# Optimization experiments

Hardware: AMD Instinct MI355X
Metric: run time of the kernel (lower is better)

## Reference

```python
import jax, jax.numpy as jnp
import numpy as np
from jax import lax

N, CIN, H, W = 128, 1024, 14, 14
CF, TH = 128, 128          # cv_filter, te_hidden
HP, GT, FP, A = 256, 256, 256, 32


def setup_inputs() -> dict:
    key = jax.random.key(0)
    ks = jax.random.split(key, 12)
    s = 0.05
    return {
        "image": jax.random.normal(ks[0], (N, CIN, H, W), jnp.float32),
        "code": jax.random.normal(ks[1], (N, TH), jnp.float32),
        "conv_w": jax.random.normal(ks[2], (CF, CIN, 3, 3), jnp.float32) * 0.02,
        "conv_b": jnp.zeros((CF,), jnp.float32),
        "hp_w0": jax.random.normal(ks[3], (CF + 2 + TH, HP), jnp.float32) * s,
        "hp_b0": jnp.zeros((HP,), jnp.float32),
        "hp_w1": jax.random.normal(ks[4], (HP, 1), jnp.float32) * s,
        "hp_b1": jnp.zeros((1,), jnp.float32),
        "gt_w0": jax.random.normal(ks[5], ((CF + 2) * 2 + TH, GT), jnp.float32) * s,
        "gt_b0": jnp.zeros((GT,), jnp.float32),
        "gt_w1": jax.random.normal(ks[6], (GT, GT), jnp.float32) * s,
        "gt_b1": jnp.zeros((GT,), jnp.float32),
        "fp_w0": jax.random.normal(ks[7], (GT, FP), jnp.float32) * s,
        "fp_b0": jnp.zeros((FP,), jnp.float32),
        "fp_w1": jax.random.normal(ks[8], (FP, A), jnp.float32) * s,
        "fp_b1": jnp.zeros((A,), jnp.float32),
    }


def _sarn(image, code, conv_w, conv_b, hp_w0, hp_b0, hp_w1, hp_b1,
          gt_w0, gt_b0, gt_w1, gt_b1, fp_w0, fp_b0, fp_w1, fp_b1):
    # visual_resize: 3x3 conv, stride 1, pad 1 (NCHW)
    x = lax.conv_general_dilated(image, conv_w, (1, 1), "SAME",
                                 dimension_numbers=("NCHW", "OIHW", "NCHW"))
    x = x + conv_b[None, :, None, None]                       # [n, cf, h, w]
    n, c, h, w = x.shape
    o = h * w
    # sarn_encode: append x/y coordinate channels and question code
    xc = jnp.broadcast_to(jnp.linspace(-1.0, 1.0, h).reshape(1, 1, h, 1), (n, 1, h, w))
    yc = jnp.broadcast_to(jnp.linspace(-1.0, 1.0, w).reshape(1, 1, 1, w), (n, 1, h, w))
    coord = jnp.concatenate([x, xc, yc], axis=1)              # [n, cf+2, h, w]
    q = jnp.broadcast_to(code[:, :, None, None], (n, code.shape[1], h, w))
    qenc = jnp.concatenate([coord, q], axis=1)                # [n, cf+2+th, h, w]
    ce = coord.reshape(n, c + 2, o).transpose(0, 2, 1)        # [n, o, cf+2]
    qe = qenc.reshape(n, -1, o).transpose(0, 2, 1)            # [n, o, cf+2+th]
    # h_psi: per-object attention logit
    a = jax.nn.relu(jnp.einsum("nod,dh->noh", qe, hp_w0) + hp_b0)
    att = jnp.einsum("noh,hk->nok", a, hp_w1) + hp_b1         # [n, o, 1]
    # sarn_pair: softmax select a single soft object, pair with every object
    sel = jax.nn.softmax(att[..., 0], axis=1)                 # [n, o]
    selected = jnp.einsum("no,nod->nd", sel, ce)              # [n, cf+2]
    pairs = jnp.concatenate(
        [qe, jnp.broadcast_to(selected[:, None, :], ce.shape)], axis=2)  # [n, o, 2*(cf+2)+th]
    # g_theta MLP + sum over objects
    g = jax.nn.relu(jnp.einsum("nop,pg->nog", pairs, gt_w0) + gt_b0)
    g = jax.nn.relu(jnp.einsum("nog,gk->nok", g, gt_w1) + gt_b1)
    relations = g.sum(axis=1)                                 # [n, gt]
    # f_phi MLP -> answer logits
    f = jax.nn.relu(relations @ fp_w0 + fp_b0)
    return f @ fp_w1 + fp_b1                                  # [n, a_size]


def reference(image, code, conv_w, conv_b, hp_w0, hp_b0, hp_w1, hp_b1,
              gt_w0, gt_b0, gt_w1, gt_b1, fp_w0, fp_b0, fp_w1, fp_b1):
    return _sarn(image, code, conv_w, conv_b, hp_w0, hp_b0, hp_w1, hp_b1,
                 gt_w0, gt_b0, gt_w1, gt_b1, fp_w0, fp_b0, fp_w1, fp_b1)
```

## Files before the change

### kernel.cpp

```cpp
#include <hip/hip_runtime.h>
#include <stdint.h>

typedef unsigned short u16;
typedef __bf16 bf16x8 __attribute__((ext_vector_type(8)));
typedef float f32x4 __attribute__((ext_vector_type(4)));

__device__ __forceinline__ u16 f2b(float f) {
  union { float f; uint32_t u; } v; v.f = f;
  uint32_t r = v.u + 0x7fffu + ((v.u >> 16) & 1u);
  return (u16)(r >> 16);
}
__device__ __forceinline__ float b2f(u16 b) {
  union { float f; uint32_t u; } v; v.u = ((uint32_t)b) << 16;
  return v.f;
}
__device__ __forceinline__ void g2l16(const void* g, void* l) {
  __builtin_amdgcn_global_load_lds(
      (const __attribute__((address_space(1))) void*)g,
      (__attribute__((address_space(3))) void*)l, 16, 0, 0);
}

#define N_SAMP 128
#define OPAD   224
#define ROWS   (N_SAMP * OPAD)
#define KQ     160

__global__ __launch_bounds__(256) void prep_weights(
    const float* __restrict__ conv_w, const float* __restrict__ hp_w0,
    const float* __restrict__ gt_w0, const float* __restrict__ gt_w1,
    const float* __restrict__ hp_b0, const float* __restrict__ code,
    u16* __restrict__ W2, u16* __restrict__ hp_w0t,
    u16* __restrict__ gt_w0t, u16* __restrict__ gt_w1t,
    float* __restrict__ biasHP) {
  int idx = blockIdx.x * 256 + threadIdx.x;
  const int nW2 = 9 * 128 * 1024;
  const int nHP = 256 * KQ;
  const int nGT0 = 256 * KQ;
  const int nGT1 = 256 * 256;
  if (idx < nW2) {
    int s = idx / 131072; int r = idx & 131071;
    int cf = r >> 10; int cin = r & 1023;
    W2[idx] = f2b(conv_w[(cf * 1024 + cin) * 9 + s]);
    return;
  }
  idx -= nW2;
  if (idx < nHP) {
    int nn = idx / KQ, kk = idx % KQ;
    hp_w0t[nn * KQ + kk] = (kk < 130) ? f2b(hp_w0[kk * 256 + nn]) : (u16)0;
    return;
  }
  idx -= nHP;
  if (idx < nGT0) {
    int nn = idx / KQ, kk = idx % KQ;
    gt_w0t[nn * KQ + kk] = (kk < 130) ? f2b(gt_w0[kk * 256 + nn]) : (u16)0;
    return;
  }
  idx -= nGT0;
  if (idx < nGT1) {
    int nn = idx >> 8, kk = idx & 255;
    gt_w1t[nn * 256 + kk] = f2b(gt_w1[kk * 256 + nn]);
    return;
  }
  idx -= nGT1;
  {
    int n = idx >> 8, t = idx & 255;
    float acc = hp_b0[t];
    for (int d = 0; d < 128; ++d)
      acc += code[n * 128 + d] * hp_w0[(130 + d) * 256 + t];
    biasHP[n * 256 + t] = acc;
  }
}

__global__ __launch_bounds__(256) void prep_img(const float* __restrict__ image,
                                                u16* __restrict__ imgT) {
  __shared__ float t[64][197];
  int n = blockIdx.x >> 4;
  int cin0 = (blockIdx.x & 15) * 64;
  const float* src = image + ((size_t)n * 1024 + cin0) * 196;
  for (int e = threadIdx.x; e < 64 * 196; e += 256) {
    int c = e / 196, sp = e % 196;
    t[c][sp] = src[c * 196 + sp];
  }
  __syncthreads();
  int w = threadIdx.x >> 6, lane = threadIdx.x & 63;
  for (int i = 0; i < 64; ++i) {
    int spg = i * 4 + w;
    int gy = spg >> 4, gx = spg & 15;
    float v = 0.f;
    if (gy >= 1 && gy <= 14 && gx >= 1 && gx <= 14) v = t[lane][(gy - 1) * 14 + (gx - 1)];
    imgT[(((size_t)(n * 256 + spg)) << 10) + cin0 + lane] = f2b(v);
  }
}

__global__ __launch_bounds__(256) void fill_qe(u16* __restrict__ qeb) {
  int idx = blockIdx.x * 256 + threadIdx.x;
  if (idx < ROWS * 8) {
    int row = idx >> 3, qd = idx & 7;
    int o = row % 224;
    ushort4 v = {0, 0, 0, 0};
    if (o < 196 && qd == 0) {
      int y = o / 14, x = o % 14;
      v.x = f2b(-1.f + 2.f * y / 13.f);
      v.y = f2b(-1.f + 2.f * x / 13.f);
    }
    *(ushort4*)(qeb + (size_t)row * KQ + 128 + qd * 4) = v;
    return;
  }
  idx -= ROWS * 8;
  int pr = idx >> 5, qd = idx & 31;
  int row = (pr / 28) * 224 + 196 + (pr % 28);
  *(ushort4*)(qeb + (size_t)row * KQ + qd * 4) = (ushort4){0, 0, 0, 0};
}

__global__ __launch_bounds__(256) void conv_gemm(
    const u16* __restrict__ imgT, const u16* __restrict__ W2,
    float* __restrict__ convAcc) {
  __shared__ __align__(16) u16 lA[112 * 64];
  __shared__ __align__(16) u16 lB[128 * 64];
  int tid = threadIdx.x, lane = tid & 63, w = tid >> 6;
  int wg = blockIdx.x;
  int xcd = wg & 7, grp = wg >> 3;
  int n = ((grp / 6) << 3) | xcd;
  int r6 = grp % 6;
  int oh = r6 / 3, ks = r6 % 3;
  int oBase = oh * 112;
  size_t nBase = (size_t)n << 8;
  int rowIn = lane >> 3;
  int cA = ((lane & 7) ^ rowIn) << 3;

  int yxA[4];
  for (int ii = 0; ii < 4; ++ii) {
    int t = w + ii * 4;
    int o = oBase + t * 8 + rowIn;
    bool valid = o < 196;
    int y = o / 14, x = o - y * 14;
    yxA[ii] = valid ? (y * 16 + x) : 0;
  }

  f32x4 acc[7][2];
#pragma unroll
  for (int mt = 0; mt < 7; ++mt)
#pragma unroll
    for (int j = 0; j < 2; ++j) acc[mt][j] = (f32x4){0.f, 0.f, 0.f, 0.f};

  int l = lane & 15, q = lane >> 4;
  for (int si = 0; si < 3; ++si) {
    int s = ks * 3 + si;
    int off = (s / 3) * 16 + (s % 3);
    const u16* Ws = W2 + ((size_t)(s * 128) << 10);
    for (int cb = 0; cb < 16; ++cb) {
      int k0 = cb << 6;
      __syncthreads();
      g2l16(imgT + ((nBase + (size_t)(yxA[0] + off)) << 10) + k0 + cA, &lA[(w) * 512]);
      g2l16(imgT + ((nBase + (size_t)(yxA[1] + off)) << 10) + k0 + cA, &lA[(w + 4) * 512]);
      g2l16(imgT + ((nBase + (size_t)(yxA[2] + off)) << 10) + k0 + cA, &lA[(w + 8) * 512]);
      if (w < 2)
        g2l16(imgT + ((nBase + (size_t)(yxA[3] + off)) << 10) + k0 + cA, &lA[(w + 12) * 512]);
#pragma unroll
      for (int ii = 0; ii < 4; ++ii) {
        int t = w + ii * 4;
        g2l16(Ws + ((size_t)(t * 8 + rowIn) << 10) + k0 + cA, &lB[t * 512]);
      }
      __syncthreads();
#pragma unroll
      for (int kk = 0; kk < 2; ++kk) {
        int co = ((((kk << 2) | q) ^ (l & 7)) << 3);
        bf16x8 af[7];
#pragma unroll
        for (int mt = 0; mt < 7; ++mt)
          af[mt] = *(const bf16x8*)&lA[(mt * 16 + l) * 64 + co];
#pragma unroll
        for (int jj = 0; jj < 2; ++jj) {
          bf16x8 bb = *(const bf16x8*)&lB[(w * 32 + jj * 16 + l) * 64 + co];
#pragma unroll
          for (int mt = 0; mt < 7; ++mt)
            acc[mt][jj] = __builtin_amdgcn_mfma_f32_16x16x32_bf16(af[mt], bb, acc[mt][jj], 0, 0, 0);
        }
      }
    }
  }
#pragma unroll
  for (int mt = 0; mt < 7; ++mt) {
    int o = oBase + mt * 16 + q * 4;
#pragma unroll
    for (int r4 = 0; r4 < 4; ++r4) {
      if (o + r4 < 196) {
        float* dst = convAcc + (size_t)(n * 224 + o + r4) * 128 + w * 32 + l;
        atomicAdd(dst, acc[mt][0][r4]);
        atomicAdd(dst + 16, acc[mt][1][r4]);
      }
    }
  }
}

__global__ __launch_bounds__(256) void conv_fix(
    const float* __restrict__ convAcc, const float* __restrict__ conv_b,
    u16* __restrict__ qeb) {
  int idx = blockIdx.x * 256 + threadIdx.x;
  int row196 = idx >> 5;
  int c0 = (idx & 31) << 2;
  int n = row196 / 196, o = row196 - n * 196;
  size_t row = (size_t)(n * 224 + o);
  const float4 v = *(const float4*)(convAcc + (row << 7) + c0);
  const float4 b = *(const float4*)(conv_b + c0);
  ushort4 pk;
  pk.x = f2b(v.x + b.x); pk.y = f2b(v.y + b.y);
  pk.z = f2b(v.z + b.z); pk.w = f2b(v.w + b.w);
  *(ushort4*)(qeb + row * KQ + c0) = pk;
}

template <int MODE, int KP, int KC>
__global__ __launch_bounds__(256) void gemm_kernel(
    const u16* __restrict__ A, const u16* __restrict__ Bt,
    const float* __restrict__ bias, const float* __restrict__ vec,
    float* __restrict__ outF, u16* __restrict__ outB) {
  __shared__ __align__(16) u16 lA[2][128 * 32];
  __shared__ __align__(16) u16 lB[2][128 * 32];
  int tid = threadIdx.x, lane = tid & 63, w = tid >> 6;
  int bx = blockIdx.x, by = blockIdx.y;
  int r0 = bx * 112;
  int cBase = by * 128;
  int kb = (((lane & 3) ^ ((lane >> 3) & 3)) << 3);
  int rA0 = r0 + w * 16 + (lane >> 2);
  int rA1 = r0 + (w + 4) * 16 + (lane >> 2);
  const u16* gA0 = A + (size_t)rA0 * KP + kb;
  const u16* gA1 = A + (size_t)rA1 * KP + kb;
  int cB0 = cBase + w * 16 + (lane >> 2);
  int cB1 = cBase + (w + 4) * 16 + (lane >> 2);
  const u16* gB0 = Bt + (size_t)cB0 * KP + kb;
  const u16* gB1 = Bt + (size_t)cB1 * KP + kb;

  f32x4 acc[7][2];
#pragma unroll
  for (int mt = 0; mt < 7; ++mt)
#pragma unroll
    for (int j = 0; j < 2; ++j) acc[mt][j] = (f32x4){0.f, 0.f, 0.f, 0.f};
  int colW = w * 32;
  int l = lane & 15, q = lane >> 4;
  int co = ((q ^ ((l >> 1) & 3)) << 3);

  auto STAGE = [&](int buf, int cb) {
    g2l16(gA0 + cb * 32, &lA[buf][w * 512]);
    g2l16(gA1 + cb * 32, &lA[buf][(w + 4) * 512]);
    g2l16(gB0 + cb * 32, &lB[buf][w * 512]);
    g2l16(gB1 + cb * 32, &lB[buf][(w + 4) * 512]);
  };

  auto COMPUTE = [&](int cur) {
    bf16x8 af[7];
#pragma unroll
    for (int mt = 0; mt < 7; ++mt)
      af[mt] = *(const bf16x8*)&lA[cur][(mt * 16 + l) * 32 + co];
#pragma unroll
    for (int j = 0; j < 2; ++j) {
      bf16x8 bfr = *(const bf16x8*)&lB[cur][(colW + j * 16 + l) * 32 + co];
#pragma unroll
      for (int mt = 0; mt < 7; ++mt)
        acc[mt][j] = __builtin_amdgcn_mfma_f32_16x16x32_bf16(af[mt], bfr, acc[mt][j], 0, 0, 0);
    }
  };

  STAGE(0, 0);
#pragma unroll
  for (int it = 0; it < KC - 1; ++it) {
    STAGE((it & 1) ^ 1, it + 1);
    asm volatile("s_waitcnt vmcnt(4)" ::: "memory");
    __builtin_amdgcn_s_barrier();
    __builtin_amdgcn_sched_barrier(0);
    COMPUTE(it & 1);
    __builtin_amdgcn_s_barrier();
    __builtin_amdgcn_sched_barrier(0);
  }
  asm volatile("s_waitcnt vmcnt(0)" ::: "memory");
  __builtin_amdgcn_s_barrier();
  __builtin_amdgcn_sched_barrier(0);
  COMPUTE((KC - 1) & 1);

  int q4 = lane >> 4, c = lane & 15;
  if (MODE == 0) {
    int n = bx >> 1;
    float attp[7][4];
#pragma unroll
    for (int mt = 0; mt < 7; ++mt)
#pragma unroll
      for (int r = 0; r < 4; ++r) attp[mt][r] = 0.f;
#pragma unroll
    for (int j = 0; j < 2; ++j) {
      int col = cBase + colW + j * 16 + c;
      float b0 = bias[n * 256 + col], w1 = vec[col];
#pragma unroll
      for (int mt = 0; mt < 7; ++mt)
#pragma unroll
        for (int r = 0; r < 4; ++r) {
          float v = fmaxf(acc[mt][j][r] + b0, 0.f);
          attp[mt][r] += v * w1;
        }
    }
#pragma unroll
    for (int mt = 0; mt < 7; ++mt)
#pragma unroll
      for (int r = 0; r < 4; ++r) {
        float p = attp[mt][r];
        p += __shfl_xor(p, 1, 64);
        p += __shfl_xor(p, 2, 64);
        p += __shfl_xor(p, 4, 64);
        p += __shfl_xor(p, 8, 64);
        if (c == 0) atomicAdd(&outF[r0 + mt * 16 + q4 * 4 + r], p);
      }
  } else if (MODE == 1) {
    int n = bx >> 1;
#pragma unroll
    for (int mt = 0; mt < 7; ++mt)
#pragma unroll
      for (int j = 0; j < 2; ++j) {
        int col = cBase + colW + j * 16 + c;
        float b = bias[n * 256 + col];
#pragma unroll
        for (int r = 0; r < 4; ++r) {
          int row = r0 + mt * 16 + q4 * 4 + r;
          outB[(size_t)row * 256 + col] = f2b(fmaxf(acc[mt][j][r] + b, 0.f));
        }
      }
  } else {
    int n = bx >> 1;
    int ob = (bx & 1) * 112;
#pragma unroll
    for (int j = 0; j < 2; ++j) {
      int col = cBase + colW + j * 16 + c;
      float b = bias[col];
      float sum = 0.f;
#pragma unroll
      for (int mt = 0; mt < 7; ++mt)
#pragma unroll
        for (int r = 0; r < 4; ++r) {
          int o = ob + mt * 16 + q4 * 4 + r;
          if (o < 196) sum += fmaxf(acc[mt][j][r] + b, 0.f);
        }
      sum += __shfl_xor(sum, 16, 64);
      sum += __shfl_xor(sum, 32, 64);
      if (q4 == 0) atomicAdd(&outF[n * 256 + col], sum);
    }
  }
}

__global__ __launch_bounds__(256) void sel_kernel(
    const float* __restrict__ att, const u16* __restrict__ qeb,
    const float* __restrict__ gt_w0, const float* __restrict__ gt_b0,
    const float* __restrict__ code, float* __restrict__ bias2) {
  int n = blockIdx.x, t = threadIdx.x;
  int w = t >> 6, lane = t & 63;
  __shared__ u16 sq[196][130];
  __shared__ float sm[196];
  __shared__ float sel[130];
  __shared__ float red[8];
  const u16* base = qeb + (size_t)n * 224 * KQ;
  for (int o = w; o < 196; o += 4) {
    const u16* rowp = base + (size_t)o * KQ;
    for (int c = lane; c < 130; c += 64) sq[o][c] = rowp[c];
  }
  float a = (t < 196) ? att[n * 224 + t] : -1e30f;
  float m = a;
  for (int mask = 1; mask < 64; mask <<= 1) m = fmaxf(m, __shfl_xor(m, mask, 64));
  if (lane == 0) red[w] = m;
  __syncthreads();
  float M = fmaxf(fmaxf(red[0], red[1]), fmaxf(red[2], red[3]));
  float e = (t < 196) ? expf(a - M) : 0.f;
  float sAcc = e;
  for (int mask = 1; mask < 64; mask <<= 1) sAcc += __shfl_xor(sAcc, mask, 64);
  if (lane == 0) red[4 + w] = sAcc;
  __syncthreads();
  float S = red[4] + red[5] + red[6] + red[7];
  if (t < 196) sm[t] = e / S;
  __syncthreads();
  if (t < 130) {
    float acc = 0.f;
    for (int o = 0; o < 196; ++o) acc += sm[o] * b2f(sq[o][t]);
    sel[t] = acc;
  }
  __syncthreads();
  float acc2 = gt_b0[t];
  for (int d = 0; d < 130; ++d) acc2 += sel[d] * gt_w0[(258 + d) * 256 + t];
  for (int d = 0; d < 128; ++d) acc2 += code[n * 128 + d] * gt_w0[(130 + d) * 256 + t];
  bias2[n * 256 + t] = acc2;
}

__global__ __launch_bounds__(256) void fphi(
    const float* __restrict__ relations, const float* __restrict__ fp_w0,
    const float* __restrict__ fp_b0, const float* __restrict__ fp_w1,
    const float* __restrict__ fp_b1, float* __restrict__ out) {
  int n = blockIdx.x, t = threadIdx.x;
  __shared__ float rel[256];
  __shared__ float f[256];
  rel[t] = relations[n * 256 + t];
  __syncthreads();
  float acc = fp_b0[t];
  for (int k = 0; k < 256; ++k) acc += rel[k] * fp_w0[k * 256 + t];
  f[t] = fmaxf(acc, 0.f);
  __syncthreads();
  if (t < 32) {
    float o = fp_b1[0];
    for (int k = 0; k < 256; ++k) o += f[k] * fp_w1[k * 32 + t];
    out[n * 32 + t] = o;
  }
}

extern "C" void kernel_launch(void* const* d_in, const int* in_sizes, int n_in,
                              void* d_out, int out_size, void* d_ws, size_t ws_size,
                              hipStream_t stream) {
  const float* image = (const float*)d_in[0];
  const float* code = (const float*)d_in[1];
  const float* conv_w = (const float*)d_in[2];
  const float* conv_b = (const float*)d_in[3];
  const float* hp_w0 = (const float*)d_in[4];
  const float* hp_b0 = (const float*)d_in[5];
  const float* hp_w1 = (const float*)d_in[6];
  const float* gt_w0 = (const float*)d_in[8];
  const float* gt_b0 = (const float*)d_in[9];
  const float* gt_w1 = (const float*)d_in[10];
  const float* gt_b1 = (const float*)d_in[11];
  const float* fp_w0 = (const float*)d_in[12];
  const float* fp_b0 = (const float*)d_in[13];
  const float* fp_w1 = (const float*)d_in[14];
  const float* fp_b1 = (const float*)d_in[15];
  float* out = (float*)d_out;

  char* p = (char*)d_ws;
  u16* imgT = (u16*)p;   p += (size_t)128 * 256 * 1024 * 2;
  u16* W2 = (u16*)p;     p += (size_t)9 * 128 * 1024 * 2;
  u16* qeb = (u16*)p;    p += (size_t)ROWS * KQ * 2;
  u16* hp_w0t = (u16*)p; p += (size_t)256 * KQ * 2;
  u16* gt_w0t = (u16*)p; p += (size_t)256 * KQ * 2;
  u16* gt_w1t = (u16*)p; p += (size_t)256 * 256 * 2;
  float* att = (float*)p;    p += (size_t)ROWS * 4;
  float* bias2 = (float*)p;  p += (size_t)128 * 256 * 4;
  float* biasHP = (float*)p; p += (size_t)128 * 256 * 4;
  float* convAcc = (float*)p; p += (size_t)ROWS * 128 * 4;
  float* relations = (float*)p; p += (size_t)128 * 256 * 4;
  u16* g1 = (u16*)convAcc;

  hipMemsetAsync(att, 0, (size_t)ROWS * 4, stream);
  hipMemsetAsync(relations, 0, (size_t)128 * 256 * 4, stream);
  hipMemsetAsync(convAcc, 0, (size_t)ROWS * 128 * 4, stream);

  prep_weights<<<5312, 256, 0, stream>>>(conv_w, hp_w0, gt_w0, gt_w1, hp_b0, code,
                                         W2, hp_w0t, gt_w0t, gt_w1t, biasHP);
  prep_img<<<2048, 256, 0, stream>>>(image, imgT);
  fill_qe<<<1344, 256, 0, stream>>>(qeb);
  conv_gemm<<<768, 256, 0, stream>>>(imgT, W2, convAcc);
  conv_fix<<<3136, 256, 0, stream>>>(convAcc, conv_b, qeb);
  gemm_kernel<0, KQ, 5><<<dim3(256, 2), 256, 0, stream>>>(qeb, hp_w0t, biasHP, hp_w1, att, nullptr);
  sel_kernel<<<128, 256, 0, stream>>>(att, qeb, gt_w0, gt_b0, code, bias2);
  gemm_kernel<1, KQ, 5><<<dim3(256, 2), 256, 0, stream>>>(qeb, gt_w0t, bias2, nullptr, nullptr, g1);
  gemm_kernel<2, 256, 8><<<dim3(256, 2), 256, 0, stream>>>(g1, gt_w1t, gt_b1, nullptr, relations, nullptr);
  fphi<<<128, 256, 0, stream>>>(relations, fp_w0, fp_b0, fp_w1, fp_b1, out);
}
```

Before: 397.0 us.

## Merge prep kernels and memsets, coalesce weight and image repacking

```diff
diff --git a/kernel.cpp b/kernel.cpp
--- a/kernel.cpp
+++ b/kernel.cpp
@@ -25,50 +25,98 @@
 #define ROWS   (N_SAMP * OPAD)
 #define KQ     160
 
-__global__ __launch_bounds__(256) void prep_weights(
-    const float* __restrict__ conv_w, const float* __restrict__ hp_w0,
-    const float* __restrict__ gt_w0, const float* __restrict__ gt_w1,
-    const float* __restrict__ hp_b0, const float* __restrict__ code,
-    u16* __restrict__ W2, u16* __restrict__ hp_w0t,
-    u16* __restrict__ gt_w0t, u16* __restrict__ gt_w1t,
-    float* __restrict__ biasHP) {
+__global__ __launch_bounds__(256) void prep_w2(const float* __restrict__ conv_w,
+                                               u16* __restrict__ W2) {
+  __shared__ float ls[2304];
+  int p0 = blockIdx.x << 8;
+  int t = threadIdx.x;
+  const float* src = conv_w + (size_t)p0 * 9;
+#pragma unroll
+  for (int i = 0; i < 9; ++i) ls[t + i * 256] = src[t + i * 256];
+  __syncthreads();
+#pragma unroll
+  for (int s = 0; s < 9; ++s)
+    W2[s * 131072 + p0 + t] = f2b(ls[t * 9 + s]);
+}
+
+#define R_HP   40960
+#define R_GT0  40960
+#define R_GT1  65536
+#define R_BHP  32768
+#define R_BGT  32768
+#define R_QC   (ROWS * 8)
+#define R_QP   114688
+#define R_ATT  7168
+#define R_REL  8192
+#define R_CVA  917504
+__global__ __launch_bounds__(256) void init_misc(
+    const float* __restrict__ hp_w0, const float* __restrict__ gt_w0,
+    const float* __restrict__ gt_w1, const float* __restrict__ hp_b0,
+    const float* __restrict__ gt_b0, const float* __restrict__ code,
+    u16* __restrict__ hp_w0t, u16* __restrict__ gt_w0t, u16* __restrict__ gt_w1t,
+    float* __restrict__ biasHP, float* __restrict__ biasGT, u16* __restrict__ qeb,
+    float* __restrict__ att, float* __restrict__ relations,
+    float* __restrict__ convAcc) {
   int idx = blockIdx.x * 256 + threadIdx.x;
-  const int nW2 = 9 * 128 * 1024;
-  const int nHP = 256 * KQ;
-  const int nGT0 = 256 * KQ;
-  const int nGT1 = 256 * 256;
-  if (idx < nW2) {
-    int s = idx / 131072; int r = idx & 131071;
-    int cf = r >> 10; int cin = r & 1023;
-    W2[idx] = f2b(conv_w[(cf * 1024 + cin) * 9 + s]);
-    return;
-  }
-  idx -= nW2;
-  if (idx < nHP) {
+  if (idx < R_HP) {
     int nn = idx / KQ, kk = idx % KQ;
-    hp_w0t[nn * KQ + kk] = (kk < 130) ? f2b(hp_w0[kk * 256 + nn]) : (u16)0;
-    return;
-  }
-  idx -= nHP;
-  if (idx < nGT0) {
+    hp_w0t[idx] = (kk < 130) ? f2b(hp_w0[kk * 256 + nn]) : (u16)0;
+    return;
+  }
+  idx -= R_HP;
+  if (idx < R_GT0) {
     int nn = idx / KQ, kk = idx % KQ;
-    gt_w0t[nn * KQ + kk] = (kk < 130) ? f2b(gt_w0[kk * 256 + nn]) : (u16)0;
-    return;
-  }
-  idx -= nGT0;
-  if (idx < nGT1) {
+    gt_w0t[idx] = (kk < 130) ? f2b(gt_w0[kk * 256 + nn]) : (u16)0;
+    return;
+  }
+  idx -= R_GT0;
+  if (idx < R_GT1) {
     int nn = idx >> 8, kk = idx & 255;
-    gt_w1t[nn * 256 + kk] = f2b(gt_w1[kk * 256 + nn]);
-    return;
-  }
-  idx -= nGT1;
-  {
+    gt_w1t[idx] = f2b(gt_w1[kk * 256 + nn]);
+    return;
+  }
+  idx -= R_GT1;
+  if (idx < R_BHP) {
     int n = idx >> 8, t = idx & 255;
     float acc = hp_b0[t];
-    for (int d = 0; d < 128; ++d)
-      acc += code[n * 128 + d] * hp_w0[(130 + d) * 256 + t];
-    biasHP[n * 256 + t] = acc;
-  }
+    for (int d = 0; d < 128; ++d) acc += code[n * 128 + d] * hp_w0[(130 + d) * 256 + t];
+    biasHP[idx] = acc;
+    return;
+  }
+  idx -= R_BHP;
+  if (idx < R_BGT) {
+    int n = idx >> 8, t = idx & 255;
+    float acc = gt_b0[t];
+    for (int d = 0; d < 128; ++d) acc += code[n * 128 + d] * gt_w0[(130 + d) * 256 + t];
+    biasGT[idx] = acc;
+    return;
+  }
+  idx -= R_BGT;
+  if (idx < R_QC) {
+    int row = idx >> 3, qd = idx & 7;
+    int o = row % 224;
+    ushort4 v = {0, 0, 0, 0};
+    if (o < 196 && qd == 0) {
+      int y = o / 14, x = o % 14;
+      v.x = f2b(-1.f + 2.f * y / 13.f);
+      v.y = f2b(-1.f + 2.f * x / 13.f);
+    }
+    *(ushort4*)(qeb + (size_t)row * KQ + 128 + qd * 4) = v;
+    return;
+  }
+  idx -= R_QC;
+  if (idx < R_QP) {
+    int pr = idx >> 5, qd = idx & 31;
+    int row = (pr / 28) * 224 + 196 + (pr % 28);
+    *(ushort4*)(qeb + (size_t)row * KQ + qd * 4) = (ushort4){0, 0, 0, 0};
+    return;
+  }
+  idx -= R_QP;
+  if (idx < R_ATT) { *((float4*)att + idx) = (float4){0.f, 0.f, 0.f, 0.f}; return; }
+  idx -= R_ATT;
+  if (idx < R_REL) { *((float4*)relations + idx) = (float4){0.f, 0.f, 0.f, 0.f}; return; }
+  idx -= R_REL;
+  *((float4*)convAcc + idx) = (float4){0.f, 0.f, 0.f, 0.f};
 }
 
 __global__ __launch_bounds__(256) void prep_img(const float* __restrict__ image,
@@ -82,34 +130,24 @@
     t[c][sp] = src[c * 196 + sp];
   }
   __syncthreads();
-  int w = threadIdx.x >> 6, lane = threadIdx.x & 63;
-  for (int i = 0; i < 64; ++i) {
-    int spg = i * 4 + w;
+#pragma unroll
+  for (int i = 0; i < 8; ++i) {
+    int qid = threadIdx.x + i * 256;
+    int spg = qid >> 3, qd = qid & 7;
     int gy = spg >> 4, gx = spg & 15;
-    float v = 0.f;
-    if (gy >= 1 && gy <= 14 && gx >= 1 && gx <= 14) v = t[lane][(gy - 1) * 14 + (gx - 1)];
-    imgT[(((size_t)(n * 256 + spg)) << 10) + cin0 + lane] = f2b(v);
-  }
-}
-
-__global__ __launch_bounds__(256) void fill_qe(u16* __restrict__ qeb) {
-  int idx = blockIdx.x * 256 + threadIdx.x;
-  if (idx < ROWS * 8) {
-    int row = idx >> 3, qd = idx & 7;
-    int o = row % 224;
-    ushort4 v = {0, 0, 0, 0};
-    if (o < 196 && qd == 0) {
-      int y = o / 14, x = o % 14;
-      v.x = f2b(-1.f + 2.f * y / 13.f);
-      v.y = f2b(-1.f + 2.f * x / 13.f);
-    }
-    *(ushort4*)(qeb + (size_t)row * KQ + 128 + qd * 4) = v;
-    return;
-  }
-  idx -= ROWS * 8;
-  int pr = idx >> 5, qd = idx & 31;
-  int row = (pr / 28) * 224 + 196 + (pr % 28);
-  *(ushort4*)(qeb + (size_t)row * KQ + qd * 4) = (ushort4){0, 0, 0, 0};
+    uint4 pk = {0u, 0u, 0u, 0u};
+    if (gy >= 1 && gy <= 14 && gx >= 1 && gx <= 14) {
+      int sp = (gy - 1) * 14 + (gx - 1);
+      uint32_t vv[8];
+#pragma unroll
+      for (int j = 0; j < 8; ++j) vv[j] = f2b(t[qd * 8 + j][sp]);
+      pk.x = vv[0] | (vv[1] << 16);
+      pk.y = vv[2] | (vv[3] << 16);
+      pk.z = vv[4] | (vv[5] << 16);
+      pk.w = vv[6] | (vv[7] << 16);
+    }
+    *(uint4*)(imgT + (((size_t)(n * 256 + spg)) << 10) + cin0 + qd * 8) = pk;
+  }
 }
 
 __global__ __launch_bounds__(256) void conv_gemm(
@@ -345,8 +383,8 @@
 
 __global__ __launch_bounds__(256) void sel_kernel(
     const float* __restrict__ att, const u16* __restrict__ qeb,
-    const float* __restrict__ gt_w0, const float* __restrict__ gt_b0,
-    const float* __restrict__ code, float* __restrict__ bias2) {
+    const float* __restrict__ gt_w0, const float* __restrict__ biasGT,
+    float* __restrict__ bias2) {
   int n = blockIdx.x, t = threadIdx.x;
   int w = t >> 6, lane = t & 63;
   __shared__ u16 sq[196][130];
@@ -378,9 +416,8 @@
     sel[t] = acc;
   }
   __syncthreads();
-  float acc2 = gt_b0[t];
+  float acc2 = biasGT[n * 256 + t];
   for (int d = 0; d < 130; ++d) acc2 += sel[d] * gt_w0[(258 + d) * 256 + t];
-  for (int d = 0; d < 128; ++d) acc2 += code[n * 128 + d] * gt_w0[(130 + d) * 256 + t];
   bias2[n * 256 + t] = acc2;
 }
 
@@ -434,22 +471,20 @@
   float* att = (float*)p;    p += (size_t)ROWS * 4;
   float* bias2 = (float*)p;  p += (size_t)128 * 256 * 4;
   float* biasHP = (float*)p; p += (size_t)128 * 256 * 4;
+  float* biasGT = (float*)p; p += (size_t)128 * 256 * 4;
   float* convAcc = (float*)p; p += (size_t)ROWS * 128 * 4;
   float* relations = (float*)p; p += (size_t)128 * 256 * 4;
   u16* g1 = (u16*)convAcc;
 
-  hipMemsetAsync(att, 0, (size_t)ROWS * 4, stream);
-  hipMemsetAsync(relations, 0, (size_t)128 * 256 * 4, stream);
-  hipMemsetAsync(convAcc, 0, (size_t)ROWS * 128 * 4, stream);
-
-  prep_weights<<<5312, 256, 0, stream>>>(conv_w, hp_w0, gt_w0, gt_w1, hp_b0, code,
-                                         W2, hp_w0t, gt_w0t, gt_w1t, biasHP);
+  init_misc<<<5820, 256, 0, stream>>>(hp_w0, gt_w0, gt_w1, hp_b0, gt_b0, code,
+                                      hp_w0t, gt_w0t, gt_w1t, biasHP, biasGT, qeb,
+                                      att, relations, convAcc);
+  prep_w2<<<512, 256, 0, stream>>>(conv_w, W2);
   prep_img<<<2048, 256, 0, stream>>>(image, imgT);
-  fill_qe<<<1344, 256, 0, stream>>>(qeb);
   conv_gemm<<<768, 256, 0, stream>>>(imgT, W2, convAcc);
   conv_fix<<<3136, 256, 0, stream>>>(convAcc, conv_b, qeb);
   gemm_kernel<0, KQ, 5><<<dim3(256, 2), 256, 0, stream>>>(qeb, hp_w0t, biasHP, hp_w1, att, nullptr);
-  sel_kernel<<<128, 256, 0, stream>>>(att, qeb, gt_w0, gt_b0, code, bias2);
+  sel_kernel<<<128, 256, 0, stream>>>(att, qeb, gt_w0, biasGT, bias2);
   gemm_kernel<1, KQ, 5><<<dim3(256, 2), 256, 0, stream>>>(qeb, gt_w0t, bias2, nullptr, nullptr, g1);
   gemm_kernel<2, 256, 8><<<dim3(256, 2), 256, 0, stream>>>(g1, gt_w1t, gt_b1, nullptr, relations, nullptr);
   fphi<<<128, 256, 0, stream>>>(relations, fp_w0, fp_b0, fp_w1, fp_b1, out);
```

After: 381.8 us. 3.8% less time.
